# Performance work log

Hardware: AMD Instinct MI355X
Metric: run time of the kernel (lower is better)

## Reference

```python
import jax, jax.numpy as jnp
import numpy as np

B, S, D, H = 2, 2048, 1024, 16
DK = D // H
THETA = 10000.0


def apply_rope(t, pos):
    # t: [B, H, S, DK], pos: [B, S] int
    half = DK // 2
    inv_freq = THETA ** (-jnp.arange(0, DK, 2, dtype=jnp.float32) / DK)  # [half]
    ang = pos.astype(jnp.float32)[:, None, :, None] * inv_freq  # [B,1,S,half]
    cos, sin = jnp.cos(ang), jnp.sin(ang)
    t1, t2 = t[..., 0::2], t[..., 1::2]  # interleaved pairs
    r1 = t1 * cos - t2 * sin
    r2 = t1 * sin + t2 * cos
    return jnp.stack([r1, r2], axis=-1).reshape(t.shape)


def setup_inputs() -> dict:
    key = jax.random.key(0)
    ks = jax.random.split(key, 5)
    x = jax.random.normal(ks[0], (B, S, D), dtype=jnp.float32)
    scale = 0.02
    Wq = jax.random.normal(ks[1], (D, D), dtype=jnp.float32) * scale
    Wk = jax.random.normal(ks[2], (D, D), dtype=jnp.float32) * scale
    Wv = jax.random.normal(ks[3], (D, D), dtype=jnp.float32) * scale
    Wo = jax.random.normal(ks[4], (D, D), dtype=jnp.float32) * scale
    token_positions = jnp.broadcast_to(jnp.arange(S, dtype=jnp.int64), (B, S))
    return {"x": x, "Wq": Wq, "Wk": Wk, "Wv": Wv, "Wo": Wo,
            "token_positions": token_positions}


def reference(x, Wq, Wk, Wv, Wo, token_positions):
    # Bias-free linear projections: y = x @ W^T (torch Linear convention)
    q = jnp.einsum('bsd,ed->bse', x, Wq)
    k = jnp.einsum('bsd,ed->bse', x, Wk)
    v = jnp.einsum('bsd,ed->bse', x, Wv)
    # split heads: [B, S, H*DK] -> [B, H, S, DK]
    def split(t):
        return t.reshape(B, S, H, DK).transpose(0, 2, 1, 3)
    qh, kh, vh = split(q), split(k), split(v)
    qh = apply_rope(qh, token_positions)
    kh = apply_rope(kh, token_positions)
    scores = jnp.einsum('bhqd,bhkd->bhqk', qh, kh) / jnp.sqrt(jnp.float32(DK))
    causal = jnp.tril(jnp.ones((S, S), dtype=bool))
    scores = jnp.where(causal, scores, jnp.finfo(scores.dtype).min)
    probs = jax.nn.softmax(scores, axis=-1)
    out = jnp.einsum('bhqk,bhkd->bhqd', probs, vh)  # [B,H,S,DK]
    out = out.transpose(0, 2, 1, 3).reshape(B, S, D)
    return jnp.einsum('bsd,ed->bse', out, Wo)
```

## Files before the change

kernel.cpp:

```cpp
#include <hip/hip_runtime.h>
#include <stdint.h>

#define B_  2
#define S_  2048
#define D_  1024
#define H_  16
#define DK_ 64

using bf16x8 = __attribute__((ext_vector_type(8))) short;
using f32x4  = __attribute__((ext_vector_type(4))) float;

__device__ __forceinline__ unsigned short f2bf(float f) {
    union { float f; uint32_t u; } v; v.f = f;
    uint32_t r = v.u + 0x7FFFu + ((v.u >> 16) & 1u);
    return (unsigned short)(r >> 16);
}

__device__ __forceinline__ uint32_t cvtpk(float lo, float hi) {
    uint32_t r;
    asm("v_cvt_pk_bf16_f32 %0, %1, %2" : "=v"(r) : "v"(lo), "v"(hi));
    return r;
}
__device__ __forceinline__ void ps32(uint32_t& a, uint32_t& b) {
    asm volatile("v_permlane32_swap_b32 %0, %1" : "+v"(a), "+v"(b));
}
__device__ __forceinline__ void ps16(uint32_t& a, uint32_t& b) {
    asm volatile("v_permlane16_swap_b32 %0, %1" : "+v"(a), "+v"(b));
}

#define GLD16(G, L) __builtin_amdgcn_global_load_lds( \
    (const __attribute__((address_space(1))) void*)(const void*)(G), \
    (__attribute__((address_space(3))) void*)(void*)(L), 16, 0, 0)

__global__ __launch_bounds__(256) void k_f32_to_bf16(const float* __restrict__ src,
                                                     unsigned short* __restrict__ dst,
                                                     int n4) {
    int i = blockIdx.x * 256 + threadIdx.x;
    if (i >= n4) return;
    float4 v = ((const float4*)src)[i];
    union { unsigned short u[4]; uint2 d; } o;
    o.u[0] = f2bf(v.x); o.u[1] = f2bf(v.y); o.u[2] = f2bf(v.z); o.u[3] = f2bf(v.w);
    ((uint2*)dst)[i] = o.d;
}

__global__ __launch_bounds__(256) void k_wconv(
    const float* __restrict__ s0, const float* __restrict__ s1,
    const float* __restrict__ s2, const float* __restrict__ s3,
    unsigned short* __restrict__ d0, unsigned short* __restrict__ d1,
    unsigned short* __restrict__ d2, unsigned short* __restrict__ d3) {
    const int w = blockIdx.y;
    const float* s = w == 0 ? s0 : w == 1 ? s1 : w == 2 ? s2 : s3;
    unsigned short* d = w == 0 ? d0 : w == 1 ? d1 : w == 2 ? d2 : d3;
    int i = blockIdx.x * 256 + threadIdx.x;
    float4 v = ((const float4*)s)[i];
    union { unsigned short u[4]; uint2 dd; } o;
    o.u[0] = f2bf(v.x); o.u[1] = f2bf(v.y); o.u[2] = f2bf(v.z); o.u[3] = f2bf(v.w);
    ((uint2*)d)[i] = o.dd;
}

template<int MODE>
__global__ __launch_bounds__(256) void k_gemm_bt(
    const unsigned short* __restrict__ A,
    const unsigned short* __restrict__ W0,
    const unsigned short* __restrict__ W1,
    const unsigned short* __restrict__ W2,
    void* __restrict__ C0, void* __restrict__ C1, void* __restrict__ C2,
    int M, int N, int K)
{
    __shared__ __align__(16) unsigned short As[128 * 32];
    __shared__ __align__(16) unsigned short Bs[128 * 32];

    const int tid  = threadIdx.x;
    const int wid  = tid >> 6, lane = tid & 63;
    const int m16  = lane & 15, g = lane >> 4;
    const int m0   = blockIdx.x * 128, n0 = blockIdx.y * 128;
    const unsigned short* Wm = blockIdx.z == 0 ? W0 : (blockIdx.z == 1 ? W1 : W2);
    void* Cm = blockIdx.z == 0 ? C0 : (blockIdx.z == 1 ? C1 : C2);

    const int wm = (wid >> 1) * 64, wn = (wid & 1) * 64;
    const int srow = lane >> 2;
    const int scol = (lane & 3) * 8;

    const f32x4 fz = {0.f, 0.f, 0.f, 0.f};
    f32x4 acc[4][4];
#pragma unroll
    for (int i = 0; i < 4; ++i)
#pragma unroll
        for (int j = 0; j < 4; ++j) acc[i][j] = fz;

    for (int k0 = 0; k0 < K; k0 += 32) {
#pragma unroll
        for (int c = 0; c < 2; ++c) {
            const int chunk = wid * 2 + c;
            const int row   = chunk * 16 + srow;
            GLD16(A  + (size_t)(m0 + row) * K + k0 + scol, As + chunk * 512);
            GLD16(Wm + (size_t)(n0 + row) * K + k0 + scol, Bs + chunk * 512);
        }
        __syncthreads();
        bf16x8 af[4], bf[4];
#pragma unroll
        for (int i = 0; i < 4; ++i)
            af[i] = *(const bf16x8*)(As + (wm + i * 16 + m16) * 32 + g * 8);
#pragma unroll
        for (int j = 0; j < 4; ++j)
            bf[j] = *(const bf16x8*)(Bs + (wn + j * 16 + m16) * 32 + g * 8);
#pragma unroll
        for (int i = 0; i < 4; ++i)
#pragma unroll
            for (int j = 0; j < 4; ++j)
                acc[i][j] = __builtin_amdgcn_mfma_f32_16x16x32_bf16(af[i], bf[j], acc[i][j], 0, 0, 0);
        __syncthreads();
    }

#pragma unroll
    for (int i = 0; i < 4; ++i) {
#pragma unroll
        for (int j = 0; j < 4; ++j) {
#pragma unroll
            for (int r = 0; r < 4; ++r) {
                const int row = m0 + wm + i * 16 + g * 4 + r;
                const int col = n0 + wn + j * 16 + m16;
                const float val = acc[i][j][r];
                if (MODE == 1) {
                    ((float*)Cm)[(size_t)row * N + col] = val;
                } else {
                    const int b = row >> 11, s = row & (S_ - 1);
                    const int h = col >> 6,  dk = col & (DK_ - 1);
                    size_t idx;
                    if (blockIdx.z == 2)
                        idx = ((size_t)((b * H_ + h) * DK_ + dk)) * S_ + s;
                    else
                        idx = ((size_t)((b * H_ + h) * S_ + s)) * DK_ + dk;
                    ((unsigned short*)Cm)[idx] = f2bf(val);
                }
            }
        }
    }
}

__global__ __launch_bounds__(256) void k_rope_inplace(
    unsigned short* __restrict__ qh, unsigned short* __restrict__ kh,
    const int* __restrict__ tok)
{
    const int idx = blockIdx.x * 256 + threadIdx.x;
    const int c = idx & 7;
    const int s = (idx >> 3) & (S_ - 1);
    const int b = idx >> 18;
    const size_t off = (size_t)idx * 8;

    const float pos = (float)tok[b * S_ + s];
    float cs[4], sn[4];
#pragma unroll
    for (int i = 0; i < 4; ++i) {
        const int p = c * 4 + i;
        const float inv = exp2f((float)(-2 * p) * (13.287712379549449f / 64.f));
        sincosf(pos * inv, &sn[i], &cs[i]);
    }
    bf16x8 qv = *(bf16x8*)(qh + off);
    bf16x8 kv = *(bf16x8*)(kh + off);
    bf16x8 qo, ko;
#pragma unroll
    for (int i = 0; i < 4; ++i) {
        union { uint32_t u; float f; } q1{(uint32_t)(unsigned short)qv[2*i] << 16};
        union { uint32_t u; float f; } q2{(uint32_t)(unsigned short)qv[2*i+1] << 16};
        qo[2 * i]     = (short)f2bf(q1.f * cs[i] - q2.f * sn[i]);
        qo[2 * i + 1] = (short)f2bf(q1.f * sn[i] + q2.f * cs[i]);
        union { uint32_t u; float f; } k1{(uint32_t)(unsigned short)kv[2*i] << 16};
        union { uint32_t u; float f; } k2{(uint32_t)(unsigned short)kv[2*i+1] << 16};
        ko[2 * i]     = (short)f2bf(k1.f * cs[i] - k2.f * sn[i]);
        ko[2 * i + 1] = (short)f2bf(k1.f * sn[i] + k2.f * cs[i]);
    }
    *(bf16x8*)(qh + off) = qo;
    *(bf16x8*)(kh + off) = ko;
}

__global__ __launch_bounds__(256, 4) void k_fattn5(
    const unsigned short* __restrict__ Q,
    const unsigned short* __restrict__ K,
    const unsigned short* __restrict__ Vt,
    unsigned short* __restrict__ O)
{
    __shared__ __align__(16) unsigned short Ks[2][64 * 64];
    __shared__ __align__(16) unsigned short Vs[2][64 * 64];

    const int tid = threadIdx.x, wid = tid >> 6, lane = tid & 63;
    const int m16 = lane & 15, g = lane >> 4;
    const int bh = blockIdx.x & 31;
    const int qg = blockIdx.x >> 5;
    const int a  = qg & 7, kq = qg >> 3;
    const int qi = kq == 0 ? a : (kq == 1 ? 15 - a : (kq == 2 ? 16 + a : 31 - a));
    const int q0 = qi * 64;
    const int qw0 = q0 + wid * 16;
    const int b = bh >> 4, h = bh & 15;
    const unsigned short* Kb = K  + (size_t)bh * S_ * DK_;
    const unsigned short* Vb = Vt + (size_t)bh * DK_ * S_;

    bf16x8 qf[2];
    {
        const unsigned short* qp = Q + (size_t)bh * S_ * DK_
                                     + (size_t)(qw0 + m16) * DK_ + g * 8;
        qf[0] = *(const bf16x8*)(qp);
        qf[1] = *(const bf16x8*)(qp + 32);
    }

    const f32x4 fz = {0.f, 0.f, 0.f, 0.f};
    f32x4 o[4];
#pragma unroll
    for (int i = 0; i < 4; ++i) o[i] = fz;
    float ps = 0.f;

    const int r8   = lane >> 3;
    const int slot = (lane & 7) ^ r8;

#pragma unroll
    for (int c = 0; c < 2; ++c) {
        const int ch = wid * 2 + c;
        GLD16(Kb + (size_t)(ch * 8 + r8) * DK_ + slot * 8, &Ks[0][ch * 512]);
        GLD16(Vb + (size_t)(ch * 8 + r8) * S_  + slot * 8, &Vs[0][ch * 512]);
    }
    __syncthreads();

    const int nt = qi + 1;
    int buf = 0;
    const float kSc = 0.125f * 1.4426950408889634f;

    for (int t = 0; t < nt; ++t) {
        const int kv0 = t * 64;
        if (t + 1 < nt) {
#pragma unroll
            for (int c = 0; c < 2; ++c) {
                const int ch = wid * 2 + c;
                GLD16(Kb + (size_t)(kv0 + 64 + ch * 8 + r8) * DK_ + slot * 8,
                      &Ks[buf ^ 1][ch * 512]);
                GLD16(Vb + (size_t)(ch * 8 + r8) * S_ + kv0 + 64 + slot * 8,
                      &Vs[buf ^ 1][ch * 512]);
            }
        }

        f32x4 sc[4];
        __builtin_amdgcn_s_setprio(1);
#pragma unroll
        for (int c = 0; c < 4; ++c) {
            const int row = c * 16 + m16, rr = row & 7;
            bf16x8 kf0 = *(const bf16x8*)(&Ks[buf][row * 64 + ((g ^ rr) << 3)]);
            bf16x8 kf1 = *(const bf16x8*)(&Ks[buf][row * 64 + (((4 + g) ^ rr) << 3)]);
            f32x4 z = fz;
            z = __builtin_amdgcn_mfma_f32_16x16x32_bf16(kf0, qf[0], z, 0, 0, 0);
            z = __builtin_amdgcn_mfma_f32_16x16x32_bf16(kf1, qf[1], z, 0, 0, 0);
            sc[c] = z;
        }
        __builtin_amdgcn_s_setprio(0);

        const bool maskT = (t == qi);
        const int qrow = qw0 + m16;
        uint32_t pk[4][2];
#pragma unroll
        for (int c = 0; c < 4; ++c) {
            float p[4];
#pragma unroll
            for (int r = 0; r < 4; ++r) {
                float v = exp2f(sc[c][r] * kSc);
                if (maskT && (kv0 + c * 16 + g * 4 + r > qrow)) v = 0.f;
                p[r] = v;
            }
            ps += (p[0] + p[1]) + (p[2] + p[3]);
            pk[c][0] = cvtpk(p[0], p[1]);
            pk[c][1] = cvtpk(p[2], p[3]);
        }

        bf16x8 pf[2];
#pragma unroll
        for (int ks = 0; ks < 2; ++ks) {
            uint32_t ylo = pk[2 * ks][0], zlo = pk[2 * ks + 1][0];
            ps32(ylo, zlo); ps16(ylo, zlo);
            uint32_t yhi = pk[2 * ks][1], zhi = pk[2 * ks + 1][1];
            ps32(yhi, zhi); ps16(yhi, zhi);
            union { uint32_t u[4]; bf16x8 v; } fu;
            fu.u[0] = ylo; fu.u[1] = yhi; fu.u[2] = zlo; fu.u[3] = zhi;
            pf[ks] = fu.v;
        }

        __builtin_amdgcn_s_setprio(1);
#pragma unroll
        for (int c2 = 0; c2 < 4; ++c2) {
            const int rv = (c2 * 16 + m16) & 7;
            bf16x8 v0 = *(const bf16x8*)(&Vs[buf][(c2 * 16 + m16) * 64 + ((g ^ rv) << 3)]);
            bf16x8 v1 = *(const bf16x8*)(&Vs[buf][(c2 * 16 + m16) * 64 + (((4 + g) ^ rv) << 3)]);
            o[c2] = __builtin_amdgcn_mfma_f32_16x16x32_bf16(pf[0], v0, o[c2], 0, 0, 0);
            o[c2] = __builtin_amdgcn_mfma_f32_16x16x32_bf16(pf[1], v1, o[c2], 0, 0, 0);
        }
        __builtin_amdgcn_s_setprio(0);

        __syncthreads();
        buf ^= 1;
    }

    float s = ps;
    s += __shfl_xor(s, 16);
    s += __shfl_xor(s, 32);
    const float inv = 1.f / s;
    float lrq[4];
#pragma unroll
    for (int r = 0; r < 4; ++r)
        lrq[r] = __shfl(inv, g * 4 + r);
#pragma unroll
    for (int c2 = 0; c2 < 4; ++c2)
#pragma unroll
        for (int r = 0; r < 4; ++r) {
            const int orow = qw0 + g * 4 + r;
            const int ocol = h * DK_ + c2 * 16 + m16;
            O[((size_t)(b * S_ + orow)) * D_ + ocol] = f2bf(o[c2][r] * lrq[r]);
        }
}

extern "C" void kernel_launch(void* const* d_in, const int* in_sizes, int n_in,
                              void* d_out, int out_size, void* d_ws, size_t ws_size,
                              hipStream_t stream) {
    (void)in_sizes; (void)n_in; (void)out_size; (void)ws_size;
    const float* x   = (const float*)d_in[0];
    const float* Wq  = (const float*)d_in[1];
    const float* Wk  = (const float*)d_in[2];
    const float* Wv  = (const float*)d_in[3];
    const float* Wo  = (const float*)d_in[4];
    const int*   tok = (const int*)d_in[5];

    char* ws = (char*)d_ws;
    const size_t MB = 1u << 20;
    unsigned short* xb  = (unsigned short*)(ws + 0 * MB);
    unsigned short* wqb = (unsigned short*)(ws + 8 * MB);
    unsigned short* wkb = (unsigned short*)(ws + 10 * MB);
    unsigned short* wvb = (unsigned short*)(ws + 12 * MB);
    unsigned short* wob = (unsigned short*)(ws + 14 * MB);
    unsigned short* qh  = (unsigned short*)(ws + 16 * MB);
    unsigned short* kh  = (unsigned short*)(ws + 24 * MB);
    unsigned short* vh  = (unsigned short*)(ws + 32 * MB);
    unsigned short* ao  = (unsigned short*)(ws + 40 * MB);

    k_f32_to_bf16<<<4096, 256, 0, stream>>>(x, xb, (B_ * S_ * D_) / 4);
    k_wconv<<<dim3(1024, 4), 256, 0, stream>>>(Wq, Wk, Wv, Wo, wqb, wkb, wvb, wob);

    k_gemm_bt<0><<<dim3(32, 8, 3), 256, 0, stream>>>(
        xb, wqb, wkb, wvb, qh, kh, vh, B_ * S_, D_, D_);

    k_rope_inplace<<<2048, 256, 0, stream>>>(qh, kh, tok);

    k_fattn5<<<dim3(1024), 256, 0, stream>>>(qh, kh, vh, ao);

    k_gemm_bt<1><<<dim3(32, 8, 1), 256, 0, stream>>>(
        ao, wob, wob, wob, d_out, d_out, d_out, B_ * S_, D_, D_);
}
```

Before: 133.8 us.

## Pair causal query tiles per block for balanced attention work

```diff
diff --git a/kernel.cpp b/kernel.cpp
--- a/kernel.cpp
+++ b/kernel.cpp
@@ -174,7 +174,7 @@
     *(bf16x8*)(kh + off) = ko;
 }
 
-__global__ __launch_bounds__(256, 4) void k_fattn5(
+__global__ __launch_bounds__(256, 2) void k_fattn6(
     const unsigned short* __restrict__ Q,
     const unsigned short* __restrict__ K,
     const unsigned short* __restrict__ Vt,
@@ -186,131 +186,137 @@
     const int tid = threadIdx.x, wid = tid >> 6, lane = tid & 63;
     const int m16 = lane & 15, g = lane >> 4;
     const int bh = blockIdx.x & 31;
-    const int qg = blockIdx.x >> 5;
-    const int a  = qg & 7, kq = qg >> 3;
-    const int qi = kq == 0 ? a : (kq == 1 ? 15 - a : (kq == 2 ? 16 + a : 31 - a));
-    const int q0 = qi * 64;
-    const int qw0 = q0 + wid * 16;
+    const int j  = blockIdx.x >> 5;
     const int b = bh >> 4, h = bh & 15;
+    const unsigned short* Qb = Q  + (size_t)bh * S_ * DK_;
     const unsigned short* Kb = K  + (size_t)bh * S_ * DK_;
     const unsigned short* Vb = Vt + (size_t)bh * DK_ * S_;
 
-    bf16x8 qf[2];
-    {
-        const unsigned short* qp = Q + (size_t)bh * S_ * DK_
-                                     + (size_t)(qw0 + m16) * DK_ + g * 8;
-        qf[0] = *(const bf16x8*)(qp);
-        qf[1] = *(const bf16x8*)(qp + 32);
-    }
-
-    const f32x4 fz = {0.f, 0.f, 0.f, 0.f};
-    f32x4 o[4];
-#pragma unroll
-    for (int i = 0; i < 4; ++i) o[i] = fz;
-    float ps = 0.f;
-
     const int r8   = lane >> 3;
     const int slot = (lane & 7) ^ r8;
-
-#pragma unroll
-    for (int c = 0; c < 2; ++c) {
-        const int ch = wid * 2 + c;
-        GLD16(Kb + (size_t)(ch * 8 + r8) * DK_ + slot * 8, &Ks[0][ch * 512]);
-        GLD16(Vb + (size_t)(ch * 8 + r8) * S_  + slot * 8, &Vs[0][ch * 512]);
-    }
+    const int ch0  = wid * 2, ch1 = wid * 2 + 1;
+
+    const f32x4 fz = {0.f, 0.f, 0.f, 0.f};
+    const float kSc = 0.125f * 1.4426950408889634f;
+
+    GLD16(Kb + (size_t)(ch0 * 8 + r8) * DK_ + slot * 8, &Ks[0][ch0 * 512]);
+    GLD16(Kb + (size_t)(ch1 * 8 + r8) * DK_ + slot * 8, &Ks[0][ch1 * 512]);
+    GLD16(Vb + (size_t)(ch0 * 8 + r8) * S_  + slot * 8, &Vs[0][ch0 * 512]);
+    GLD16(Vb + (size_t)(ch1 * 8 + r8) * S_  + slot * 8, &Vs[0][ch1 * 512]);
     __syncthreads();
 
-    const int nt = qi + 1;
     int buf = 0;
-    const float kSc = 0.125f * 1.4426950408889634f;
-
-    for (int t = 0; t < nt; ++t) {
-        const int kv0 = t * 64;
-        if (t + 1 < nt) {
-#pragma unroll
-            for (int c = 0; c < 2; ++c) {
-                const int ch = wid * 2 + c;
-                GLD16(Kb + (size_t)(kv0 + 64 + ch * 8 + r8) * DK_ + slot * 8,
-                      &Ks[buf ^ 1][ch * 512]);
-                GLD16(Vb + (size_t)(ch * 8 + r8) * S_ + kv0 + 64 + slot * 8,
-                      &Vs[buf ^ 1][ch * 512]);
-            }
+#pragma unroll
+    for (int ph = 0; ph < 2; ++ph) {
+        const int qi = ph ? 31 - j : j;
+        const int q0 = qi * 64;
+        const int qw0 = q0 + wid * 16;
+
+        bf16x8 qf[2];
+        {
+            const unsigned short* qp = Qb + (size_t)(qw0 + m16) * DK_ + g * 8;
+            qf[0] = *(const bf16x8*)(qp);
+            qf[1] = *(const bf16x8*)(qp + 32);
         }
 
-        f32x4 sc[4];
-        __builtin_amdgcn_s_setprio(1);
-#pragma unroll
-        for (int c = 0; c < 4; ++c) {
-            const int row = c * 16 + m16, rr = row & 7;
-            bf16x8 kf0 = *(const bf16x8*)(&Ks[buf][row * 64 + ((g ^ rr) << 3)]);
-            bf16x8 kf1 = *(const bf16x8*)(&Ks[buf][row * 64 + (((4 + g) ^ rr) << 3)]);
-            f32x4 z = fz;
-            z = __builtin_amdgcn_mfma_f32_16x16x32_bf16(kf0, qf[0], z, 0, 0, 0);
-            z = __builtin_amdgcn_mfma_f32_16x16x32_bf16(kf1, qf[1], z, 0, 0, 0);
-            sc[c] = z;
+        f32x4 o[4];
+#pragma unroll
+        for (int i = 0; i < 4; ++i) o[i] = fz;
+        float ps = 0.f;
+
+        const int nt = qi + 1;
+        for (int t = 0; t < nt; ++t) {
+            const int kv0 = t * 64;
+            int nkv0 = -1;
+            if (t + 1 < nt)      nkv0 = kv0 + 64;
+            else if (ph == 0)    nkv0 = 0;
+            if (nkv0 >= 0) {
+                GLD16(Kb + (size_t)(nkv0 + ch0 * 8 + r8) * DK_ + slot * 8, &Ks[buf ^ 1][ch0 * 512]);
+                GLD16(Kb + (size_t)(nkv0 + ch1 * 8 + r8) * DK_ + slot * 8, &Ks[buf ^ 1][ch1 * 512]);
+                GLD16(Vb + (size_t)(ch0 * 8 + r8) * S_ + nkv0 + slot * 8, &Vs[buf ^ 1][ch0 * 512]);
+                GLD16(Vb + (size_t)(ch1 * 8 + r8) * S_ + nkv0 + slot * 8, &Vs[buf ^ 1][ch1 * 512]);
+            }
+
+            f32x4 sc[4];
+            __builtin_amdgcn_s_setprio(1);
+#pragma unroll
+            for (int c = 0; c < 4; ++c) {
+                const int row = c * 16 + m16, rr = row & 7;
+                bf16x8 kf0 = *(const bf16x8*)(&Ks[buf][row * 64 + ((g ^ rr) << 3)]);
+                bf16x8 kf1 = *(const bf16x8*)(&Ks[buf][row * 64 + (((4 + g) ^ rr) << 3)]);
+                f32x4 z = fz;
+                z = __builtin_amdgcn_mfma_f32_16x16x32_bf16(kf0, qf[0], z, 0, 0, 0);
+                z = __builtin_amdgcn_mfma_f32_16x16x32_bf16(kf1, qf[1], z, 0, 0, 0);
+                sc[c] = z;
+            }
+            __builtin_amdgcn_s_setprio(0);
+
+            bf16x8 vf[2][4];
+#pragma unroll
+            for (int c2 = 0; c2 < 4; ++c2) {
+                const int rv = (c2 * 16 + m16) & 7;
+                vf[0][c2] = *(const bf16x8*)(&Vs[buf][(c2 * 16 + m16) * 64 + ((g ^ rv) << 3)]);
+                vf[1][c2] = *(const bf16x8*)(&Vs[buf][(c2 * 16 + m16) * 64 + (((4 + g) ^ rv) << 3)]);
+            }
+
+            const bool maskT = (t == qi);
+            const int qrow = qw0 + m16;
+            uint32_t pk[4][2];
+#pragma unroll
+            for (int c = 0; c < 4; ++c) {
+                float p[4];
+#pragma unroll
+                for (int r = 0; r < 4; ++r) {
+                    float v = exp2f(sc[c][r] * kSc);
+                    if (maskT && (kv0 + c * 16 + g * 4 + r > qrow)) v = 0.f;
+                    p[r] = v;
+                }
+                ps += (p[0] + p[1]) + (p[2] + p[3]);
+                pk[c][0] = cvtpk(p[0], p[1]);
+                pk[c][1] = cvtpk(p[2], p[3]);
+            }
+
+            bf16x8 pf[2];
+#pragma unroll
+            for (int ks = 0; ks < 2; ++ks) {
+                uint32_t ylo = pk[2 * ks][0], zlo = pk[2 * ks + 1][0];
+                ps32(ylo, zlo); ps16(ylo, zlo);
+                uint32_t yhi = pk[2 * ks][1], zhi = pk[2 * ks + 1][1];
+                ps32(yhi, zhi); ps16(yhi, zhi);
+                union { uint32_t u[4]; bf16x8 v; } fu;
+                fu.u[0] = ylo; fu.u[1] = yhi; fu.u[2] = zlo; fu.u[3] = zhi;
+                pf[ks] = fu.v;
+            }
+
+            __builtin_amdgcn_s_setprio(1);
+#pragma unroll
+            for (int c2 = 0; c2 < 4; ++c2) {
+                o[c2] = __builtin_amdgcn_mfma_f32_16x16x32_bf16(pf[0], vf[0][c2], o[c2], 0, 0, 0);
+                o[c2] = __builtin_amdgcn_mfma_f32_16x16x32_bf16(pf[1], vf[1][c2], o[c2], 0, 0, 0);
+            }
+            __builtin_amdgcn_s_setprio(0);
+
+            __syncthreads();
+            buf ^= 1;
         }
-        __builtin_amdgcn_s_setprio(0);
-
-        const bool maskT = (t == qi);
-        const int qrow = qw0 + m16;
-        uint32_t pk[4][2];
-#pragma unroll
-        for (int c = 0; c < 4; ++c) {
-            float p[4];
+
+        float s = ps;
+        s += __shfl_xor(s, 16);
+        s += __shfl_xor(s, 32);
+        const float inv = 1.f / s;
+        float lrq[4];
+#pragma unroll
+        for (int r = 0; r < 4; ++r)
+            lrq[r] = __shfl(inv, g * 4 + r);
+#pragma unroll
+        for (int c2 = 0; c2 < 4; ++c2)
 #pragma unroll
             for (int r = 0; r < 4; ++r) {
-                float v = exp2f(sc[c][r] * kSc);
-                if (maskT && (kv0 + c * 16 + g * 4 + r > qrow)) v = 0.f;
-                p[r] = v;
-            }
-            ps += (p[0] + p[1]) + (p[2] + p[3]);
-            pk[c][0] = cvtpk(p[0], p[1]);
-            pk[c][1] = cvtpk(p[2], p[3]);
-        }
-
-        bf16x8 pf[2];
-#pragma unroll
-        for (int ks = 0; ks < 2; ++ks) {
-            uint32_t ylo = pk[2 * ks][0], zlo = pk[2 * ks + 1][0];
-            ps32(ylo, zlo); ps16(ylo, zlo);
-            uint32_t yhi = pk[2 * ks][1], zhi = pk[2 * ks + 1][1];
-            ps32(yhi, zhi); ps16(yhi, zhi);
-            union { uint32_t u[4]; bf16x8 v; } fu;
-            fu.u[0] = ylo; fu.u[1] = yhi; fu.u[2] = zlo; fu.u[3] = zhi;
-            pf[ks] = fu.v;
-        }
-
-        __builtin_amdgcn_s_setprio(1);
-#pragma unroll
-        for (int c2 = 0; c2 < 4; ++c2) {
-            const int rv = (c2 * 16 + m16) & 7;
-            bf16x8 v0 = *(const bf16x8*)(&Vs[buf][(c2 * 16 + m16) * 64 + ((g ^ rv) << 3)]);
-            bf16x8 v1 = *(const bf16x8*)(&Vs[buf][(c2 * 16 + m16) * 64 + (((4 + g) ^ rv) << 3)]);
-            o[c2] = __builtin_amdgcn_mfma_f32_16x16x32_bf16(pf[0], v0, o[c2], 0, 0, 0);
-            o[c2] = __builtin_amdgcn_mfma_f32_16x16x32_bf16(pf[1], v1, o[c2], 0, 0, 0);
-        }
-        __builtin_amdgcn_s_setprio(0);
-
-        __syncthreads();
-        buf ^= 1;
-    }
-
-    float s = ps;
-    s += __shfl_xor(s, 16);
-    s += __shfl_xor(s, 32);
-    const float inv = 1.f / s;
-    float lrq[4];
-#pragma unroll
-    for (int r = 0; r < 4; ++r)
-        lrq[r] = __shfl(inv, g * 4 + r);
-#pragma unroll
-    for (int c2 = 0; c2 < 4; ++c2)
-#pragma unroll
-        for (int r = 0; r < 4; ++r) {
-            const int orow = qw0 + g * 4 + r;
-            const int ocol = h * DK_ + c2 * 16 + m16;
-            O[((size_t)(b * S_ + orow)) * D_ + ocol] = f2bf(o[c2][r] * lrq[r]);
-        }
+                const int orow = qw0 + g * 4 + r;
+                const int ocol = h * DK_ + c2 * 16 + m16;
+                O[((size_t)(b * S_ + orow)) * D_ + ocol] = f2bf(o[c2][r] * lrq[r]);
+            }
+    }
 }
 
 extern "C" void kernel_launch(void* const* d_in, const int* in_sizes, int n_in,
@@ -344,7 +350,7 @@
 
     k_rope_inplace<<<2048, 256, 0, stream>>>(qh, kh, tok);
 
-    k_fattn5<<<dim3(1024), 256, 0, stream>>>(qh, kh, vh, ao);
+    k_fattn6<<<dim3(512), 256, 0, stream>>>(qh, kh, vh, ao);
 
     k_gemm_bt<1><<<dim3(32, 8, 1), 256, 0, stream>>>(
         ao, wob, wob, wob, d_out, d_out, d_out, B_ * S_, D_, D_);
```

After: 130.4 us. -2.5%, faster.
